# Kernel optimization log

Hardware: AMD Instinct MI355X
Metric: run time of the kernel (lower is better)

Reference implementation:

```python
import jax, jax.numpy as jnp
import numpy as np

GROUP_SIZE = 128
LORA_SCALING = 32.0 / 16.0  # lora_alpha / r


def _unpack_rows(q):
    # q: int32 [n, m] -> uint4 values [n*8, m], 8 nibbles per int32 along axis 0
    shifts = (jnp.arange(8, dtype=jnp.int32) * 4)
    vals = (q[:, None, :] >> shifts[None, :, None]) & 0xF
    return vals.reshape(q.shape[0] * 8, q.shape[1])


def _unpack_cols(q):
    # q: int32 [g, m] -> uint4 values [g, m*8], 8 nibbles per int32 along axis 1
    shifts = (jnp.arange(8, dtype=jnp.int32) * 4)
    vals = (q[:, :, None] >> shifts[None, None, :]) & 0xF
    return vals.reshape(q.shape[0], q.shape[1] * 8)


def setup_inputs() -> dict:
    key = jax.random.key(0)
    ks = jax.random.split(key, 6)
    in_f, out_f, tokens, r = 4096, 11008, 64, 16
    g = in_f // GROUP_SIZE  # 32 groups
    x = jax.random.normal(ks[0], (tokens, in_f), dtype=jnp.float32)
    qweight = jax.random.randint(ks[1], (in_f // 8, out_f), jnp.iinfo(jnp.int32).min, jnp.iinfo(jnp.int32).max, dtype=jnp.int32)
    qzeros = jax.random.randint(ks[2], (g, out_f // 8), jnp.iinfo(jnp.int32).min, jnp.iinfo(jnp.int32).max, dtype=jnp.int32)
    scales = jax.random.uniform(ks[3], (g, out_f), dtype=jnp.float32) * 0.01 + 0.001
    lora_A = jax.random.normal(ks[4], (r, in_f), dtype=jnp.float32) * 0.02
    lora_B = jax.random.normal(ks[5], (out_f, r), dtype=jnp.float32) * 0.02
    return {"x": x, "qweight": qweight, "qzeros": qzeros, "scales": scales,
            "lora_A": lora_A, "lora_B": lora_B}


def reference(x, qweight, qzeros, scales, lora_A, lora_B):
    in_f = qweight.shape[0] * 8
    # --- GPTQ int4 dequant ---
    wq = _unpack_rows(qweight).astype(jnp.float32)          # [in, out]
    zeros = (_unpack_cols(qzeros) + 1).astype(jnp.float32)  # [groups, out] (GPTQ +1 offset)
    g_idx = jnp.arange(in_f) // GROUP_SIZE                  # [in]
    W = scales[g_idx] * (wq - zeros[g_idx])                 # [in, out]
    # base quantized matmul
    result = x @ W                                          # [tokens, out]
    # --- LoRA adapter (single active adapter, dropout=0, tmp_weight=1) ---
    lora_out = (x @ lora_A.T) @ lora_B.T                    # [tokens, out]
    return result + lora_out * LORA_SCALING
```

## Files before the change

### kernel.cpp

```cpp
#include <hip/hip_runtime.h>
#include <stdint.h>

#define TOKENS 64
#define IN_F   4096
#define OUT_F  11008
#define RANK   16
#define GS     128
#define NG     32
#define ZCOLS  (OUT_F / 8)
#define LORA_SCALE 2.0f
#define BN 32

using short8  = __attribute__((ext_vector_type(8))) short;
using float4v = __attribute__((ext_vector_type(4))) float;

static __device__ inline uint16_t f2bf(float f, float* back) {
    uint32_t u = __float_as_uint(f);
    uint32_t r = (u + 0x7FFFu + ((u >> 16) & 1u)) >> 16;
    *back = __uint_as_float(r << 16);
    return (uint16_t)r;
}

__global__ __launch_bounds__(256) void prep_kernel(
        const float* __restrict__ x,
        const float* __restrict__ loraA,
        uint4* __restrict__ xf4,
        float* __restrict__ xsumT,
        float* __restrict__ midT) {
    __shared__ float redg[256];
    __shared__ float redm[4][16];
    const int t    = blockIdx.x;
    const int tid  = threadIdx.x;
    const int lane = tid & 63;
    const int wv   = tid >> 6;

    float4 xv[4];
    const float4* xp = (const float4*)(x + (size_t)t * IN_F + tid * 16);
    #pragma unroll
    for (int i = 0; i < 4; ++i) xv[i] = xp[i];

    union { uint16_t u[16]; uint4 q[2]; } ob;
    float s = 0.f;
    #pragma unroll
    for (int i = 0; i < 4; ++i) {
        float b;
        ob.u[i * 4 + 0] = f2bf(xv[i].x, &b); s += b;
        ob.u[i * 4 + 1] = f2bf(xv[i].y, &b); s += b;
        ob.u[i * 4 + 2] = f2bf(xv[i].z, &b); s += b;
        ob.u[i * 4 + 3] = f2bf(xv[i].w, &b); s += b;
    }
    {
        const int mm = t >> 4, nn = t & 15;
        const int kchunk = tid >> 1;
        #pragma unroll
        for (int i = 0; i < 2; ++i) {
            const int qd = (tid * 2 + i) & 3;
            xf4[(size_t)((mm * 128 + kchunk) * 64 + qd * 16 + nn)] = ob.q[i];
        }
    }
    redg[tid] = s;

    float pj[16];
    #pragma unroll
    for (int j = 0; j < 16; ++j) {
        const float4* ap = (const float4*)(loraA + (size_t)j * IN_F + tid * 16);
        float ps = 0.f;
        #pragma unroll
        for (int i = 0; i < 4; ++i) {
            float4 a = ap[i];
            ps += a.x * xv[i].x + a.y * xv[i].y + a.z * xv[i].z + a.w * xv[i].w;
        }
        pj[j] = ps;
    }
    #pragma unroll
    for (int j = 0; j < 16; ++j) {
        #pragma unroll
        for (int off = 32; off; off >>= 1) pj[j] += __shfl_down(pj[j], off);
    }
    if (lane == 0) {
        #pragma unroll
        for (int j = 0; j < 16; ++j) redm[wv][j] = pj[j];
    }
    __syncthreads();
    if (tid < NG) {
        float g = 0.f;
        #pragma unroll
        for (int i = 0; i < 8; ++i) g += redg[tid * 8 + i];
        xsumT[tid * TOKENS + t] = g;
    }
    if (tid < 16)
        midT[tid * TOKENS + t] = redm[0][tid] + redm[1][tid] + redm[2][tid] + redm[3][tid];
}

#define LOAD_GROUP(g, A, B, S0, S1, Z0, Z1) do {                               \
    _Pragma("unroll")                                                          \
    for (int ks = 0; ks < 4; ++ks) A[ks] = xfw[((g) * 4 + ks) * 64];           \
    _Pragma("unroll")                                                          \
    for (int ks = 0; ks < 4; ++ks) {                                           \
        B[ks * 2]     = qwc[(size_t)((g) * 16 + ks * 4 + quad) * OUT_F];       \
        B[ks * 2 + 1] = qwc[(size_t)((g) * 16 + ks * 4 + quad) * OUT_F + 16];  \
    }                                                                          \
    S0 = scales[(size_t)(g) * OUT_F + col0 + n];                               \
    S1 = scales[(size_t)(g) * OUT_F + col0 + 16 + n];                          \
    Z0 = qz[(size_t)(g) * ZCOLS + ((col0 + n) >> 3)];                          \
    Z1 = qz[(size_t)(g) * ZCOLS + ((col0 + 16 + n) >> 3)];                     \
} while (0)

#define COMPUTE_GROUP(g, A, B, S0, S1, Z0, Z1) do {                            \
    float4v accg0 = (float4v){0.f, 0.f, 0.f, 0.f};                             \
    float4v accg1 = (float4v){0.f, 0.f, 0.f, 0.f};                             \
    _Pragma("unroll")                                                          \
    for (int ks = 0; ks < 4; ++ks) {                                           \
        union { uint4 u; short8 s; } afu; afu.u = A[ks];                       \
        _Pragma("unroll")                                                      \
        for (int nh = 0; nh < 2; ++nh) {                                       \
            uint32_t q  = B[ks * 2 + nh];                                      \
            uint32_t lo = q & 0x0F0F0F0Fu;                                     \
            uint32_t hi = (q >> 4) & 0x0F0F0F0Fu;                              \
            union { uint32_t u32[4]; short8 s8; } bf;                          \
            _Pragma("unroll")                                                  \
            for (int i = 0; i < 4; ++i)                                        \
                bf.u32[i] = __builtin_amdgcn_perm(hi, lo,                      \
                                0x0C040C00u + i * 0x00010001u) | 0x43004300u;  \
            if (nh == 0)                                                       \
                accg0 = __builtin_amdgcn_mfma_f32_16x16x32_bf16(afu.s, bf.s8,  \
                                                                accg0, 0, 0, 0);\
            else                                                               \
                accg1 = __builtin_amdgcn_mfma_f32_16x16x32_bf16(afu.s, bf.s8,  \
                                                                accg1, 0, 0, 0);\
        }                                                                      \
    }                                                                          \
    const float zoff0 = (float)(((Z0 >> (((col0 + n) & 7) * 4)) & 0xFu) + 129u);\
    const float zoff1 = (float)(((Z1 >> (((col0 + 16 + n) & 7) * 4)) & 0xFu) + 129u);\
    const float4v xv = *(const float4v*)&xsl[(g) * 64 + m * 16 + quad * 4];    \
    _Pragma("unroll")                                                          \
    for (int r = 0; r < 4; ++r) {                                              \
        acc[0][r] = fmaf(S0, fmaf(-zoff0, xv[r], accg0[r]), acc[0][r]);        \
        acc[1][r] = fmaf(S1, fmaf(-zoff1, xv[r], accg1[r]), acc[1][r]);        \
    }                                                                          \
} while (0)

__global__ __launch_bounds__(256) void main_kernel(
        const uint32_t* __restrict__ qw,
        const uint32_t* __restrict__ qz,
        const float* __restrict__ scales,
        const uint4* __restrict__ xf4,
        const float* __restrict__ xsumT,
        const float* __restrict__ midT,
        const float* __restrict__ loraB,
        float* __restrict__ out) {
    __shared__ float xsl[NG * 64];
    __shared__ float mids[16 * 64];

    const int tid  = threadIdx.x;
    const int m    = tid >> 6;
    const int lane = tid & 63;
    const int n    = lane & 15;
    const int quad = lane >> 4;
    const int col0 = blockIdx.x * BN;

    #pragma unroll
    for (int i = 0; i < 8; ++i) xsl[i * 256 + tid] = xsumT[i * 256 + tid];
    #pragma unroll
    for (int i = 0; i < 4; ++i) mids[i * 256 + tid] = midT[i * 256 + tid];
    __syncthreads();

    const uint4*    xfw = xf4 + (size_t)m * 128 * 64 + lane;
    const uint32_t* qwc = qw + col0 + n;

    float4v acc[2];
    acc[0] = (float4v){0.f, 0.f, 0.f, 0.f};
    acc[1] = (float4v){0.f, 0.f, 0.f, 0.f};

    uint4 A0[4], A1[4];
    uint32_t B0[8], B1[8];
    float S00, S01, S10, S11;
    uint32_t Z00, Z01, Z10, Z11;

    LOAD_GROUP(0, A0, B0, S00, S01, Z00, Z01);
    #pragma unroll 1
    for (int gp = 0; gp < 16; ++gp) {
        const int g0 = gp * 2;
        LOAD_GROUP(g0 + 1, A1, B1, S10, S11, Z10, Z11);
        COMPUTE_GROUP(g0, A0, B0, S00, S01, Z00, Z01);
        if (gp < 15) LOAD_GROUP(g0 + 2, A0, B0, S00, S01, Z00, Z01);
        COMPUTE_GROUP(g0 + 1, A1, B1, S10, S11, Z10, Z11);
    }

    #pragma unroll
    for (int nh = 0; nh < 2; ++nh) {
        const int col = col0 + nh * 16 + n;
        float4 lb[4];
        const float4* lbp = (const float4*)(loraB + (size_t)col * RANK);
        #pragma unroll
        for (int i = 0; i < 4; ++i) lb[i] = lbp[i];
        float4v ls = (float4v){0.f, 0.f, 0.f, 0.f};
        #pragma unroll
        for (int j = 0; j < 16; ++j) {
            const float lbj = ((const float*)lb)[j];
            const float4v mv = *(const float4v*)&mids[j * 64 + m * 16 + quad * 4];
            #pragma unroll
            for (int r = 0; r < 4; ++r) ls[r] = fmaf(mv[r], lbj, ls[r]);
        }
        #pragma unroll
        for (int r = 0; r < 4; ++r) {
            const int t = m * 16 + quad * 4 + r;
            out[(size_t)t * OUT_F + col] = acc[nh][r] + LORA_SCALE * ls[r];
        }
    }
}

extern "C" void kernel_launch(void* const* d_in, const int* in_sizes, int n_in,
                              void* d_out, int out_size, void* d_ws, size_t ws_size,
                              hipStream_t stream) {
    const float*    x      = (const float*)d_in[0];
    const uint32_t* qw     = (const uint32_t*)d_in[1];
    const uint32_t* qz     = (const uint32_t*)d_in[2];
    const float*    scales = (const float*)d_in[3];
    const float*    loraA  = (const float*)d_in[4];
    const float*    loraB  = (const float*)d_in[5];
    float* out = (float*)d_out;

    uint4* xf4   = (uint4*)d_ws;
    float* xsumT = (float*)((char*)d_ws + (size_t)TOKENS * IN_F * 2);
    float* midT  = xsumT + NG * TOKENS;

    prep_kernel<<<TOKENS, 256, 0, stream>>>(x, loraA, xf4, xsumT, midT);
    main_kernel<<<OUT_F / BN, 256, 0, stream>>>(qw, qz, scales, xf4, xsumT, midT, loraB, out);
}
```

Baseline: 108.9 us.

## Deepen weight prefetch to four stages and drop LDS staging of xsum/mid

The main loop now keeps a 4-deep ring of quantized-weight registers and a 2-deep ring for activations, scales and zeros, prefetching groups several iterations ahead instead of simple double buffering. The shared-memory staging of xsumT and midT, along with its barrier, is removed; those values are read directly from global memory (likely L2/L1 hits) inside the loop and the LoRA epilogue. This is meant to hide more HBM latency on the weight stream and cut the prologue and sync cost. In exchange it uses more registers, which may lower occupancy, and the tail iterations redundantly reload the last group.

Measured after the change: 115.4 us. +5.9%, slower.

```diff
diff --git a/kernel.cpp b/kernel.cpp
--- a/kernel.cpp
+++ b/kernel.cpp
@@ -92,29 +92,33 @@
         midT[tid * TOKENS + t] = redm[0][tid] + redm[1][tid] + redm[2][tid] + redm[3][tid];
 }
 
-#define LOAD_GROUP(g, A, B, S0, S1, Z0, Z1) do {                               \
-    _Pragma("unroll")                                                          \
-    for (int ks = 0; ks < 4; ++ks) A[ks] = xfw[((g) * 4 + ks) * 64];           \
+#define LOADB(sb, g) do {                                                      \
     _Pragma("unroll")                                                          \
     for (int ks = 0; ks < 4; ++ks) {                                           \
-        B[ks * 2]     = qwc[(size_t)((g) * 16 + ks * 4 + quad) * OUT_F];       \
-        B[ks * 2 + 1] = qwc[(size_t)((g) * 16 + ks * 4 + quad) * OUT_F + 16];  \
+        B[sb][ks * 2]     = qwc[(size_t)((g) * 16 + ks * 4 + quad) * OUT_F];   \
+        B[sb][ks * 2 + 1] = qwc[(size_t)((g) * 16 + ks * 4 + quad) * OUT_F + 16];\
     }                                                                          \
-    S0 = scales[(size_t)(g) * OUT_F + col0 + n];                               \
-    S1 = scales[(size_t)(g) * OUT_F + col0 + 16 + n];                          \
-    Z0 = qz[(size_t)(g) * ZCOLS + ((col0 + n) >> 3)];                          \
-    Z1 = qz[(size_t)(g) * ZCOLS + ((col0 + 16 + n) >> 3)];                     \
 } while (0)
 
-#define COMPUTE_GROUP(g, A, B, S0, S1, Z0, Z1) do {                            \
+#define LOADA(sa, g) do {                                                      \
+    _Pragma("unroll")                                                          \
+    for (int ks = 0; ks < 4; ++ks) A[sa][ks] = xfw[((g) * 4 + ks) * 64];       \
+    XS[sa] = *(const float4*)(xsumT + (g) * 64 + m * 16 + quad * 4);           \
+    S0[sa] = scales[(size_t)(g) * OUT_F + col0 + n];                           \
+    S1[sa] = scales[(size_t)(g) * OUT_F + col0 + 16 + n];                      \
+    Z0[sa] = qz[(size_t)(g) * ZCOLS + ((col0 + n) >> 3)];                      \
+    Z1[sa] = qz[(size_t)(g) * ZCOLS + ((col0 + 16 + n) >> 3)];                 \
+} while (0)
+
+#define COMPUTE(sa, sb) do {                                                   \
     float4v accg0 = (float4v){0.f, 0.f, 0.f, 0.f};                             \
     float4v accg1 = (float4v){0.f, 0.f, 0.f, 0.f};                             \
     _Pragma("unroll")                                                          \
     for (int ks = 0; ks < 4; ++ks) {                                           \
-        union { uint4 u; short8 s; } afu; afu.u = A[ks];                       \
+        union { uint4 u; short8 s; } afu; afu.u = A[sa][ks];                   \
         _Pragma("unroll")                                                      \
         for (int nh = 0; nh < 2; ++nh) {                                       \
-            uint32_t q  = B[ks * 2 + nh];                                      \
+            uint32_t q  = B[sb][ks * 2 + nh];                                  \
             uint32_t lo = q & 0x0F0F0F0Fu;                                     \
             uint32_t hi = (q >> 4) & 0x0F0F0F0Fu;                              \
             union { uint32_t u32[4]; short8 s8; } bf;                          \
@@ -130,13 +134,14 @@
                                                                 accg1, 0, 0, 0);\
         }                                                                      \
     }                                                                          \
-    const float zoff0 = (float)(((Z0 >> (((col0 + n) & 7) * 4)) & 0xFu) + 129u);\
-    const float zoff1 = (float)(((Z1 >> (((col0 + 16 + n) & 7) * 4)) & 0xFu) + 129u);\
-    const float4v xv = *(const float4v*)&xsl[(g) * 64 + m * 16 + quad * 4];    \
+    const float zoff0 = (float)(((Z0[sa] >> (((col0 + n) & 7) * 4)) & 0xFu) + 129u);\
+    const float zoff1 = (float)(((Z1[sa] >> (((col0 + 16 + n) & 7) * 4)) & 0xFu) + 129u);\
+    const float4 xvv = XS[sa];                                                 \
+    const float xvr[4] = {xvv.x, xvv.y, xvv.z, xvv.w};                         \
     _Pragma("unroll")                                                          \
     for (int r = 0; r < 4; ++r) {                                              \
-        acc[0][r] = fmaf(S0, fmaf(-zoff0, xv[r], accg0[r]), acc[0][r]);        \
-        acc[1][r] = fmaf(S1, fmaf(-zoff1, xv[r], accg1[r]), acc[1][r]);        \
+        acc[0][r] = fmaf(S0[sa], fmaf(-zoff0, xvr[r], accg0[r]), acc[0][r]);   \
+        acc[1][r] = fmaf(S1[sa], fmaf(-zoff1, xvr[r], accg1[r]), acc[1][r]);   \
     }                                                                          \
 } while (0)
 
@@ -149,9 +154,6 @@
         const float* __restrict__ midT,
         const float* __restrict__ loraB,
         float* __restrict__ out) {
-    __shared__ float xsl[NG * 64];
-    __shared__ float mids[16 * 64];
-
     const int tid  = threadIdx.x;
     const int m    = tid >> 6;
     const int lane = tid & 63;
@@ -159,12 +161,6 @@
     const int quad = lane >> 4;
     const int col0 = blockIdx.x * BN;
 
-    #pragma unroll
-    for (int i = 0; i < 8; ++i) xsl[i * 256 + tid] = xsumT[i * 256 + tid];
-    #pragma unroll
-    for (int i = 0; i < 4; ++i) mids[i * 256 + tid] = midT[i * 256 + tid];
-    __syncthreads();
-
     const uint4*    xfw = xf4 + (size_t)m * 128 * 64 + lane;
     const uint32_t* qwc = qw + col0 + n;
 
@@ -172,19 +168,23 @@
     acc[0] = (float4v){0.f, 0.f, 0.f, 0.f};
     acc[1] = (float4v){0.f, 0.f, 0.f, 0.f};
 
-    uint4 A0[4], A1[4];
-    uint32_t B0[8], B1[8];
-    float S00, S01, S10, S11;
-    uint32_t Z00, Z01, Z10, Z11;
-
-    LOAD_GROUP(0, A0, B0, S00, S01, Z00, Z01);
-    #pragma unroll 1
-    for (int gp = 0; gp < 16; ++gp) {
-        const int g0 = gp * 2;
-        LOAD_GROUP(g0 + 1, A1, B1, S10, S11, Z10, Z11);
-        COMPUTE_GROUP(g0, A0, B0, S00, S01, Z00, Z01);
-        if (gp < 15) LOAD_GROUP(g0 + 2, A0, B0, S00, S01, Z00, Z01);
-        COMPUTE_GROUP(g0 + 1, A1, B1, S10, S11, Z10, Z11);
+    uint32_t B[4][8];
+    uint4    A[2][4];
+    float4   XS[2];
+    float    S0[2], S1[2];
+    uint32_t Z0[2], Z1[2];
+
+    LOADB(0, 0); LOADB(1, 1); LOADB(2, 2); LOADB(3, 3);
+    LOADA(0, 0); LOADA(1, 1);
+
+    #pragma unroll 4
+    for (int g = 0; g < NG; ++g) {
+        const int sb = g & 3, sa = g & 1;
+        COMPUTE(sa, sb);
+        int gb = g + 4; if (gb > NG - 1) gb = NG - 1;
+        int ga = g + 2; if (ga > NG - 1) ga = NG - 1;
+        LOADB(sb, gb);
+        LOADA(sa, ga);
     }
 
     #pragma unroll
@@ -198,9 +198,11 @@
         #pragma unroll
         for (int j = 0; j < 16; ++j) {
             const float lbj = ((const float*)lb)[j];
-            const float4v mv = *(const float4v*)&mids[j * 64 + m * 16 + quad * 4];
-            #pragma unroll
-            for (int r = 0; r < 4; ++r) ls[r] = fmaf(mv[r], lbj, ls[r]);
+            const float4 mv = *(const float4*)(midT + j * 64 + m * 16 + quad * 4);
+            ls[0] = fmaf(mv.x, lbj, ls[0]);
+            ls[1] = fmaf(mv.y, lbj, ls[1]);
+            ls[2] = fmaf(mv.z, lbj, ls[2]);
+            ls[3] = fmaf(mv.w, lbj, ls[3]);
         }
         #pragma unroll
         for (int r = 0; r < 4; ++r) {
```

## Split K across blocks with atomics and move LoRA output to separate kernel

Applied to the files above, without the earlier changes.

The main GEMM is split into four K segments per 64-column block, and partial sums are accumulated into the output with float atomicAdd. This multiplies the grid from 344 to 688 blocks, and each wave now covers two M tiles so each dequantized weight fragment is reused across more MFMAs. A new kernel writes the LoRA term to the output first, initializing it before the atomics. The trade-offs are an extra launch, atomic traffic on the 64x11008 output, and a summation order that is no longer deterministic.

Result: no change. 107.2 us (-1.6%).

```diff
diff --git a/kernel.cpp b/kernel.cpp
--- a/kernel.cpp
+++ b/kernel.cpp
@@ -9,7 +9,6 @@
 #define NG     32
 #define ZCOLS  (OUT_F / 8)
 #define LORA_SCALE 2.0f
-#define BN 32
 
 using short8  = __attribute__((ext_vector_type(8))) short;
 using float4v = __attribute__((ext_vector_type(4))) float;
@@ -92,122 +91,149 @@
         midT[tid * TOKENS + t] = redm[0][tid] + redm[1][tid] + redm[2][tid] + redm[3][tid];
 }
 
-#define LOAD_GROUP(g, A, B, S0, S1, Z0, Z1) do {                               \
-    _Pragma("unroll")                                                          \
-    for (int ks = 0; ks < 4; ++ks) A[ks] = xfw[((g) * 4 + ks) * 64];           \
-    _Pragma("unroll")                                                          \
-    for (int ks = 0; ks < 4; ++ks) {                                           \
-        B[ks * 2]     = qwc[(size_t)((g) * 16 + ks * 4 + quad) * OUT_F];       \
-        B[ks * 2 + 1] = qwc[(size_t)((g) * 16 + ks * 4 + quad) * OUT_F + 16];  \
-    }                                                                          \
-    S0 = scales[(size_t)(g) * OUT_F + col0 + n];                               \
-    S1 = scales[(size_t)(g) * OUT_F + col0 + 16 + n];                          \
-    Z0 = qz[(size_t)(g) * ZCOLS + ((col0 + n) >> 3)];                          \
-    Z1 = qz[(size_t)(g) * ZCOLS + ((col0 + 16 + n) >> 3)];                     \
+__global__ __launch_bounds__(256) void lora_out_kernel(
+        const float* __restrict__ midT,
+        const float* __restrict__ loraB,
+        float* __restrict__ out) {
+    const int gid = blockIdx.x * 256 + threadIdx.x;
+    const int t = gid / OUT_F;
+    const int o = gid - t * OUT_F;
+    const float4* b4 = (const float4*)(loraB + (size_t)o * RANK);
+    float s = 0.f;
+    #pragma unroll
+    for (int i = 0; i < 4; ++i) {
+        float4 b = b4[i];
+        s += b.x * midT[(i * 4 + 0) * TOKENS + t];
+        s += b.y * midT[(i * 4 + 1) * TOKENS + t];
+        s += b.z * midT[(i * 4 + 2) * TOKENS + t];
+        s += b.w * midT[(i * 4 + 3) * TOKENS + t];
+    }
+    out[gid] = s * LORA_SCALE;
+}
+
+#define LOADG(st, g) do {                                                       \
+    _Pragma("unroll")                                                           \
+    for (int mt = 0; mt < 2; ++mt)                                              \
+        _Pragma("unroll")                                                       \
+        for (int ks = 0; ks < 4; ++ks)                                          \
+            A[st][mt * 4 + ks] =                                                \
+                xf4[(size_t)(((mh * 2 + mt) * 128 + (g) * 4 + ks) * 64) + lane];\
+    _Pragma("unroll")                                                           \
+    for (int ks = 0; ks < 4; ++ks)                                              \
+        _Pragma("unroll")                                                       \
+        for (int nh = 0; nh < 2; ++nh)                                          \
+            B[st][ks * 2 + nh] =                                                \
+                qwc[(size_t)((g) * 16 + ks * 4 + quad) * OUT_F + nh * 16];      \
+    _Pragma("unroll")                                                           \
+    for (int mt = 0; mt < 2; ++mt)                                              \
+        XS[st][mt] = *(const float4*)(xsumT + (g) * 64 +                        \
+                                      (mh * 2 + mt) * 16 + quad * 4);           \
+    _Pragma("unroll")                                                           \
+    for (int nh = 0; nh < 2; ++nh) {                                            \
+        S[st][nh] = scales[(size_t)(g) * OUT_F + col0 + nh * 16 + n];           \
+        Z[st][nh] = qz[(size_t)(g) * ZCOLS + ((col0 + nh * 16 + n) >> 3)];      \
+    }                                                                           \
 } while (0)
 
-#define COMPUTE_GROUP(g, A, B, S0, S1, Z0, Z1) do {                            \
-    float4v accg0 = (float4v){0.f, 0.f, 0.f, 0.f};                             \
-    float4v accg1 = (float4v){0.f, 0.f, 0.f, 0.f};                             \
-    _Pragma("unroll")                                                          \
-    for (int ks = 0; ks < 4; ++ks) {                                           \
-        union { uint4 u; short8 s; } afu; afu.u = A[ks];                       \
-        _Pragma("unroll")                                                      \
-        for (int nh = 0; nh < 2; ++nh) {                                       \
-            uint32_t q  = B[ks * 2 + nh];                                      \
-            uint32_t lo = q & 0x0F0F0F0Fu;                                     \
-            uint32_t hi = (q >> 4) & 0x0F0F0F0Fu;                              \
-            union { uint32_t u32[4]; short8 s8; } bf;                          \
-            _Pragma("unroll")                                                  \
-            for (int i = 0; i < 4; ++i)                                        \
-                bf.u32[i] = __builtin_amdgcn_perm(hi, lo,                      \
-                                0x0C040C00u + i * 0x00010001u) | 0x43004300u;  \
-            if (nh == 0)                                                       \
-                accg0 = __builtin_amdgcn_mfma_f32_16x16x32_bf16(afu.s, bf.s8,  \
-                                                                accg0, 0, 0, 0);\
-            else                                                               \
-                accg1 = __builtin_amdgcn_mfma_f32_16x16x32_bf16(afu.s, bf.s8,  \
-                                                                accg1, 0, 0, 0);\
-        }                                                                      \
-    }                                                                          \
-    const float zoff0 = (float)(((Z0 >> (((col0 + n) & 7) * 4)) & 0xFu) + 129u);\
-    const float zoff1 = (float)(((Z1 >> (((col0 + 16 + n) & 7) * 4)) & 0xFu) + 129u);\
-    const float4v xv = *(const float4v*)&xsl[(g) * 64 + m * 16 + quad * 4];    \
-    _Pragma("unroll")                                                          \
-    for (int r = 0; r < 4; ++r) {                                              \
-        acc[0][r] = fmaf(S0, fmaf(-zoff0, xv[r], accg0[r]), acc[0][r]);        \
-        acc[1][r] = fmaf(S1, fmaf(-zoff1, xv[r], accg1[r]), acc[1][r]);        \
-    }                                                                          \
+#define COMPUTEG(st) do {                                                       \
+    float4v accg[2][2];                                                         \
+    _Pragma("unroll")                                                           \
+    for (int mt = 0; mt < 2; ++mt)                                              \
+        _Pragma("unroll")                                                       \
+        for (int nh = 0; nh < 2; ++nh)                                          \
+            accg[mt][nh] = (float4v){0.f, 0.f, 0.f, 0.f};                       \
+    _Pragma("unroll")                                                           \
+    for (int ks = 0; ks < 4; ++ks) {                                            \
+        union { uint4 u; short8 s; } af0, af1;                                  \
+        af0.u = A[st][ks];                                                      \
+        af1.u = A[st][4 + ks];                                                  \
+        _Pragma("unroll")                                                       \
+        for (int nh = 0; nh < 2; ++nh) {                                        \
+            uint32_t q  = B[st][ks * 2 + nh];                                   \
+            uint32_t lo = q & 0x0F0F0F0Fu;                                      \
+            uint32_t hi = (q >> 4) & 0x0F0F0F0Fu;                               \
+            union { uint32_t u32[4]; short8 s8; } bf;                           \
+            _Pragma("unroll")                                                   \
+            for (int i = 0; i < 4; ++i)                                         \
+                bf.u32[i] = __builtin_amdgcn_perm(hi, lo,                       \
+                                0x0C040C00u + i * 0x00010001u) | 0x43004300u;   \
+            accg[0][nh] = __builtin_amdgcn_mfma_f32_16x16x32_bf16(af0.s, bf.s8, \
+                                                            accg[0][nh], 0, 0, 0);\
+            accg[1][nh] = __builtin_amdgcn_mfma_f32_16x16x32_bf16(af1.s, bf.s8, \
+                                                            accg[1][nh], 0, 0, 0);\
+        }                                                                       \
+    }                                                                           \
+    _Pragma("unroll")                                                           \
+    for (int nh = 0; nh < 2; ++nh) {                                            \
+        const float zoff = (float)(((Z[st][nh] >>                               \
+                        (((col0 + nh * 16 + n) & 7) * 4)) & 0xFu) + 129u);      \
+        const float scl = S[st][nh];                                            \
+        _Pragma("unroll")                                                       \
+        for (int mt = 0; mt < 2; ++mt) {                                        \
+            const float xr[4] = {XS[st][mt].x, XS[st][mt].y,                    \
+                                 XS[st][mt].z, XS[st][mt].w};                   \
+            _Pragma("unroll")                                                   \
+            for (int r = 0; r < 4; ++r)                                         \
+                acc[mt][nh][r] = fmaf(scl, fmaf(-zoff, xr[r],                   \
+                                      accg[mt][nh][r]), acc[mt][nh][r]);        \
+        }                                                                       \
+    }                                                                           \
 } while (0)
 
-__global__ __launch_bounds__(256) void main_kernel(
+__global__ __launch_bounds__(256, 3) void main_kernel(
         const uint32_t* __restrict__ qw,
         const uint32_t* __restrict__ qz,
         const float* __restrict__ scales,
         const uint4* __restrict__ xf4,
         const float* __restrict__ xsumT,
-        const float* __restrict__ midT,
-        const float* __restrict__ loraB,
         float* __restrict__ out) {
-    __shared__ float xsl[NG * 64];
-    __shared__ float mids[16 * 64];
-
     const int tid  = threadIdx.x;
-    const int m    = tid >> 6;
+    const int wv   = tid >> 6;
     const int lane = tid & 63;
     const int n    = lane & 15;
     const int quad = lane >> 4;
-    const int col0 = blockIdx.x * BN;
-
-    #pragma unroll
-    for (int i = 0; i < 8; ++i) xsl[i * 256 + tid] = xsumT[i * 256 + tid];
-    #pragma unroll
-    for (int i = 0; i < 4; ++i) mids[i * 256 + tid] = midT[i * 256 + tid];
-    __syncthreads();
-
-    const uint4*    xfw = xf4 + (size_t)m * 128 * 64 + lane;
+    const int mh   = wv & 1;
+    const int cs   = wv >> 1;
+    const int colblk = blockIdx.x >> 2;
+    const int kseg   = blockIdx.x & 3;
+    const int col0   = colblk * 64 + cs * 32;
+    const int g0     = kseg * 8;
+
     const uint32_t* qwc = qw + col0 + n;
 
-    float4v acc[2];
-    acc[0] = (float4v){0.f, 0.f, 0.f, 0.f};
-    acc[1] = (float4v){0.f, 0.f, 0.f, 0.f};
-
-    uint4 A0[4], A1[4];
-    uint32_t B0[8], B1[8];
-    float S00, S01, S10, S11;
-    uint32_t Z00, Z01, Z10, Z11;
-
-    LOAD_GROUP(0, A0, B0, S00, S01, Z00, Z01);
-    #pragma unroll 1
-    for (int gp = 0; gp < 16; ++gp) {
-        const int g0 = gp * 2;
-        LOAD_GROUP(g0 + 1, A1, B1, S10, S11, Z10, Z11);
-        COMPUTE_GROUP(g0, A0, B0, S00, S01, Z00, Z01);
-        if (gp < 15) LOAD_GROUP(g0 + 2, A0, B0, S00, S01, Z00, Z01);
-        COMPUTE_GROUP(g0 + 1, A1, B1, S10, S11, Z10, Z11);
-    }
-
-    #pragma unroll
-    for (int nh = 0; nh < 2; ++nh) {
-        const int col = col0 + nh * 16 + n;
-        float4 lb[4];
-        const float4* lbp = (const float4*)(loraB + (size_t)col * RANK);
-        #pragma unroll
-        for (int i = 0; i < 4; ++i) lb[i] = lbp[i];
-        float4v ls = (float4v){0.f, 0.f, 0.f, 0.f};
-        #pragma unroll
-        for (int j = 0; j < 16; ++j) {
-            const float lbj = ((const float*)lb)[j];
-            const float4v mv = *(const float4v*)&mids[j * 64 + m * 16 + quad * 4];
+    float4v acc[2][2];
+    #pragma unroll
+    for (int mt = 0; mt < 2; ++mt)
+        #pragma unroll
+        for (int nh = 0; nh < 2; ++nh)
+            acc[mt][nh] = (float4v){0.f, 0.f, 0.f, 0.f};
+
+    uint4    A[2][8];
+    uint32_t B[2][8];
+    float4   XS[2][2];
+    float    S[2][2];
+    uint32_t Z[2][2];
+
+    LOADG(0, g0);
+    LOADG(1, g0 + 1);
+    #pragma unroll
+    for (int gi = 0; gi < 8; ++gi) {
+        const int st = gi & 1;
+        COMPUTEG(st);
+        int gl = gi + 2; if (gl > 7) gl = 7;
+        LOADG(st, g0 + gl);
+    }
+
+    #pragma unroll
+    for (int mt = 0; mt < 2; ++mt)
+        #pragma unroll
+        for (int nh = 0; nh < 2; ++nh)
             #pragma unroll
-            for (int r = 0; r < 4; ++r) ls[r] = fmaf(mv[r], lbj, ls[r]);
-        }
-        #pragma unroll
-        for (int r = 0; r < 4; ++r) {
-            const int t = m * 16 + quad * 4 + r;
-            out[(size_t)t * OUT_F + col] = acc[nh][r] + LORA_SCALE * ls[r];
-        }
-    }
+            for (int r = 0; r < 4; ++r) {
+                const int t = (mh * 2 + mt) * 16 + quad * 4 + r;
+                atomicAdd(out + (size_t)t * OUT_F + col0 + nh * 16 + n,
+                          acc[mt][nh][r]);
+            }
 }
 
 extern "C" void kernel_launch(void* const* d_in, const int* in_sizes, int n_in,
@@ -226,5 +252,6 @@
     float* midT  = xsumT + NG * TOKENS;
 
     prep_kernel<<<TOKENS, 256, 0, stream>>>(x, loraA, xf4, xsumT, midT);
-    main_kernel<<<OUT_F / BN, 256, 0, stream>>>(qw, qz, scales, xf4, xsumT, midT, loraB, out);
-}
+    lora_out_kernel<<<(TOKENS * OUT_F) / 256, 256, 0, stream>>>(midT, loraB, out);
+    main_kernel<<<(OUT_F / 64) * 4, 256, 0, stream>>>(qw, qz, scales, xf4, xsumT, out);
+}
```
